# Kernel tuning notes

Measured on AMD Instinct MI355X. Metric: run time of the kernel, lower is better.

## Reference

```python
import jax, jax.numpy as jnp
import numpy as np

B, T = 2, 5            # num_frames MUST equal 5 (Embedding(5, channel) pos table)
C, CTX_C, DH = 384, 128, 64   # channel, context_channel, dim_head (lucidrains default, heads=1)
HW = [(80, 80), (40, 40), (20, 20), (10, 10)]
NS = 4
SCALE = DH ** -0.5


def _xavier(k, shape):
    fan_out, fan_in = shape[-2], shape[-1]
    lim = (6.0 / (fan_in + fan_out)) ** 0.5
    return jax.random.uniform(k, shape, jnp.float32, -lim, lim)


def setup_inputs() -> dict:
    key = jax.random.key(0)
    ks = iter(jax.random.split(key, 40))
    inp = {}
    for i, (h, w) in enumerate(HW):
        inp[f"fmap{i}"] = jax.random.normal(next(ks), (B * T, C, h, w), jnp.float32)
        inp[f"pos{i}"] = jax.random.normal(next(ks), (B, T, C, h, w), jnp.float32)
        inp[f"audio{i}"] = jax.random.normal(next(ks), (B * T, CTX_C), jnp.float32)
    inp["ctx_proj_w"] = _xavier(next(ks), (NS, C, CTX_C))
    inp["ctx_proj_b"] = jnp.zeros((NS, C), jnp.float32)
    inp["pos_emb"] = jax.random.normal(next(ks), (NS, 5, C), jnp.float32)  # Embedding(5, channel) per stage
    inp["qk_w"] = _xavier(next(ks), (NS, DH, C))
    inp["ctx_qk_w"] = _xavier(next(ks), (NS, DH, C))
    inp["v_w"] = _xavier(next(ks), (NS, DH, C))
    inp["ctx_v_w"] = _xavier(next(ks), (NS, DH, C))
    inp["out_w"] = _xavier(next(ks), (NS, C, DH))
    inp["out_b"] = jnp.zeros((NS, C), jnp.float32)
    inp["ctx_out_w"] = _xavier(next(ks), (NS, C, DH))
    inp["ctx_out_b"] = jnp.zeros((NS, C), jnp.float32)
    inp["batch_size"] = B
    inp["num_frames"] = T
    return inp


def _stage(x, pos, audio, Wp, bp, pe, Wqk, Wcqk, Wv, Wcv, Wo, bo, Wco, bco, batch_size):
    bt, c, h, w = x.shape
    # audio projection 128 -> 384
    a = audio @ Wp.T + bp                                  # (bt, C)
    # 'hw' reshape: tokens = H*W per (batch*frame)
    xf = x.reshape(bt, c, h * w).transpose(0, 2, 1)        # (bt, hw, C)
    vp = pos.reshape(bt, c, h * w).transpose(0, 2, 1)      # (bt, hw, C)
    ctx = a[:, None, :]                                    # (bt, 1, C)
    cp = jnp.tile(pe, (batch_size, 1))[:, None, :]         # (bt, 1, C); bt == 5*batch_size
    # bidirectional cross-attention (heads=1), pos added to QK inputs only
    qk = (xf + vp) @ Wqk.T                                 # (bt, hw, DH)
    v = xf @ Wv.T                                          # (bt, hw, DH)
    cqk = (ctx + cp) @ Wcqk.T                              # (bt, 1, DH)
    cv = ctx @ Wcv.T                                       # (bt, 1, DH)
    sim = jnp.einsum('bid,bjd->bij', qk, cqk) * SCALE      # (bt, hw, 1) shared similarity
    attn = jax.nn.softmax(sim, axis=-1)                    # video attends over context (j)
    ctx_attn = jax.nn.softmax(sim, axis=-2)                # context attends over video (i)
    out = jnp.einsum('bij,bjd->bid', attn, cv) @ Wo.T + bo         # (bt, hw, C)
    ctx_out = jnp.einsum('bij,bid->bjd', ctx_attn, v) @ Wco.T + bco  # (bt, 1, C)
    vout = out.transpose(0, 2, 1).reshape(bt, c, h, w)
    aout = ctx_out[:, 0, :]                                # (bt, C)
    return vout, aout


def reference(fmap0, fmap1, fmap2, fmap3, audio0, audio1, audio2, audio3,
              pos0, pos1, pos2, pos3,
              ctx_proj_w, ctx_proj_b, pos_emb, qk_w, ctx_qk_w, v_w, ctx_v_w,
              out_w, out_b, ctx_out_w, ctx_out_b, batch_size, num_frames):
    fmaps = (fmap0, fmap1, fmap2, fmap3)
    poss = (pos0, pos1, pos2, pos3)
    audios = (audio0, audio1, audio2, audio3)
    vouts, aouts = [], []
    for i in range(NS):
        vo, ao = _stage(fmaps[i], poss[i], audios[i],
                        ctx_proj_w[i], ctx_proj_b[i], pos_emb[i],
                        qk_w[i], ctx_qk_w[i], v_w[i], ctx_v_w[i],
                        out_w[i], out_b[i], ctx_out_w[i], ctx_out_b[i], batch_size)
        vouts.append(vo)
        aouts.append(ao)
    return tuple(vouts) + tuple(aouts)
```

## Files before the change

kernel.cpp:

```cpp
#include <hip/hip_runtime.h>

#define BT 10
#define CC 384
#define DH 64
#define CTXC 128
#define NS 4
#define SCALE_F 0.125f

#define VOFF0 0
#define VOFF1 24576000
#define VOFF2 30720000
#define VOFF3 32256000
#define AOUT_OFF 32640000

struct Params {
  const float* fmap0; const float* fmap1; const float* fmap2; const float* fmap3;
  const float* pos0;  const float* pos1;  const float* pos2;  const float* pos3;
  const float* audio0;const float* audio1;const float* audio2;const float* audio3;
  const float* ctx_proj_w; const float* ctx_proj_b; const float* pos_emb;
  const float* qk_w; const float* ctx_qk_w; const float* v_w; const float* ctx_v_w;
  const float* out_w; const float* out_b; const float* ctx_out_w; const float* ctx_out_b;
  float* out;
  float* r;
  float* outvec;
  float* xw;
  float* simbuf;
};

__device__ __forceinline__ int hw_of(int s){ return s==0?6400: s==1?1600: s==2?400:100; }
__device__ __forceinline__ int simoff(int s){ return s==0?0: s==1?64000: s==2?80000:84000; }
__device__ __forceinline__ const float* fm_of(const Params& P, int s){ return s==0?P.fmap0: s==1?P.fmap1: s==2?P.fmap2:P.fmap3; }
__device__ __forceinline__ const float* po_of(const Params& P, int s){ return s==0?P.pos0: s==1?P.pos1: s==2?P.pos2:P.pos3; }
__device__ __forceinline__ const float* au_of(const Params& P, int s){ return s==0?P.audio0: s==1?P.audio1: s==2?P.audio2:P.audio3; }

__global__ __launch_bounds__(384) void k_pre(Params P) {
  const int s = blockIdx.x / BT, b = blockIdx.x % BT;
  const int tid = threadIdx.x;
  __shared__ float aud[CTXC], ctxv[CC], ctxpe[CC], cqk[DH], cvv[DH];
  const float* audio = au_of(P, s);
  if (tid < CTXC) aud[tid] = audio[b*CTXC + tid];
  __syncthreads();
  {
    float acc = P.ctx_proj_b[s*CC + tid];
    const float* wrow = P.ctx_proj_w + (size_t)(s*CC + tid)*CTXC;
    #pragma unroll 8
    for (int k = 0; k < CTXC; ++k) acc += wrow[k]*aud[k];
    ctxv[tid] = acc;
    ctxpe[tid] = acc + P.pos_emb[(s*5 + (b%5))*CC + tid];
  }
  __syncthreads();
  if (tid < DH) {
    float q = 0.f, v = 0.f;
    const float* wq = P.ctx_qk_w + (size_t)(s*DH + tid)*CC;
    const float* wv = P.ctx_v_w  + (size_t)(s*DH + tid)*CC;
    #pragma unroll 4
    for (int c = 0; c < CC; ++c) { q += wq[c]*ctxpe[c]; v += wv[c]*ctxv[c]; }
    cqk[tid] = q; cvv[tid] = v;
  }
  __syncthreads();
  {
    float rr = 0.f, ov = P.out_b[s*CC + tid];
    const float* wqk = P.qk_w + (size_t)s*DH*CC + tid;
    const float* wo  = P.out_w + (size_t)(s*CC + tid)*DH;
    #pragma unroll 4
    for (int d = 0; d < DH; ++d) { rr += wqk[(size_t)d*CC]*cqk[d]; ov += wo[d]*cvv[d]; }
    P.r[(s*BT+b)*CC + tid] = rr * SCALE_F;
    P.outvec[(s*BT+b)*CC + tid] = ov;
  }
}

__global__ __launch_bounds__(256) void k_sim(Params P) {
  const int bid = blockIdx.x;
  int s, b, chunk, part, HW;
  if (bid < 560)      { s=0; int l=bid;     b=l/56; int r2=l%56; chunk=r2>>3; part=r2&7; HW=6400; }
  else if (bid < 720) { s=1; int l=bid-560; b=l/16; int r2=l%16; chunk=r2>>3; part=r2&7; HW=1600; }
  else if (bid < 800) { s=2; int l=bid-720; b=l>>3; part=l&7; chunk=0; HW=400; }
  else                { s=3; int l=bid-800; b=l>>3; part=l&7; chunk=0; HW=100; }
  const int tid = threadIdx.x;
  const int c0 = part*48;
  const int hw4 = HW >> 2;

  __shared__ float rs[48];
  if (tid < 48) rs[tid] = P.r[(s*BT+b)*CC + c0 + tid];
  __syncthreads();

  const int i4 = chunk*256 + tid;
  if (i4 < hw4) {
    const float4* xp = (const float4*)(fm_of(P, s) + ((size_t)b*CC + c0)*HW) + i4;
    const float4* pp = (const float4*)(po_of(P, s) + ((size_t)b*CC + c0)*HW) + i4;
    float4 acc = {0.f, 0.f, 0.f, 0.f};
    #pragma unroll 8
    for (int c = 0; c < 48; ++c) {
      const float4 x = xp[(size_t)c*hw4];
      const float4 p = pp[(size_t)c*hw4];
      const float rc = rs[c];
      acc.x += (x.x + p.x) * rc;
      acc.y += (x.y + p.y) * rc;
      acc.z += (x.z + p.z) * rc;
      acc.w += (x.w + p.w) * rc;
    }
    float* dst = P.simbuf + simoff(s) + b*HW + i4*4;
    atomicAdd(dst + 0, acc.x);
    atomicAdd(dst + 1, acc.y);
    atomicAdd(dst + 2, acc.z);
    atomicAdd(dst + 3, acc.w);
  }
}

__global__ __launch_bounds__(256) void k_softmax(Params P) {
  const int s = blockIdx.x / BT, b = blockIdx.x % BT;
  const int HW = hw_of(s);
  float* sim = P.simbuf + simoff(s) + b*HW;
  const int tid = threadIdx.x;
  const int wid = tid >> 6, lane = tid & 63;
  __shared__ float red[4], red2[4];

  float m = -1e30f;
  for (int i = tid; i < HW; i += 256) m = fmaxf(m, sim[i]);
  #pragma unroll
  for (int off = 32; off; off >>= 1) m = fmaxf(m, __shfl_down(m, off));
  if (lane == 0) red[wid] = m;
  __syncthreads();
  if (tid == 0) { float mm = red[0]; for (int w2 = 1; w2 < 4; ++w2) mm = fmaxf(mm, red[w2]); red[0] = mm; }
  __syncthreads();
  m = red[0];

  float sum = 0.f;
  for (int i = tid; i < HW; i += 256) { float e = expf(sim[i] - m); sim[i] = e; sum += e; }
  #pragma unroll
  for (int off = 32; off; off >>= 1) sum += __shfl_down(sum, off);
  if (lane == 0) red2[wid] = sum;
  __syncthreads();
  if (tid == 0) { float ss = red2[0]; for (int w2 = 1; w2 < 4; ++w2) ss += red2[w2]; red2[0] = ss; }
  __syncthreads();
  const float invS = 1.f / red2[0];

  for (int i = tid; i < HW; i += 256) sim[i] *= invS;
}

__global__ __launch_bounds__(256) void k_xw(Params P) {
  const int bid = blockIdx.x;
  const int sb = bid / 96, ct = bid % 96;
  const int s = sb / BT, b = sb % BT;
  const int HW = hw_of(s);
  const int wid = threadIdx.x >> 6, lane = threadIdx.x & 63;
  const int c = ct*4 + wid;
  const float* xrow = fm_of(P, s) + ((size_t)(b*CC + c))*HW;
  const float* wrow = P.simbuf + simoff(s) + b*HW;
  float ax=0.f, ay=0.f, az=0.f, aw=0.f;
  #pragma unroll 4
  for (int i0 = lane*4; i0 < HW; i0 += 256) {
    const float4 x4 = *(const float4*)(xrow + i0);
    const float4 w4 = *(const float4*)(wrow + i0);
    ax += x4.x*w4.x; ay += x4.y*w4.y; az += x4.z*w4.z; aw += x4.w*w4.w;
  }
  float acc = (ax + ay) + (az + aw);
  #pragma unroll
  for (int off = 32; off; off >>= 1) acc += __shfl_down(acc, off);
  if (lane == 0) P.xw[(s*BT+b)*CC + c] = acc;
}

__global__ __launch_bounds__(384) void k_post(Params P) {
  const int s = blockIdx.x / BT, b = blockIdx.x % BT;
  const int tid = threadIdx.x;
  __shared__ float xws[CC], ctxo[DH];
  xws[tid] = P.xw[(s*BT+b)*CC + tid];
  __syncthreads();
  if (tid < DH) {
    float acc = 0.f;
    const float* wv = P.v_w + (size_t)(s*DH + tid)*CC;
    #pragma unroll 4
    for (int c = 0; c < CC; ++c) acc += wv[c]*xws[c];
    ctxo[tid] = acc;
  }
  __syncthreads();
  float ao = P.ctx_out_b[s*CC + tid];
  const float* wco = P.ctx_out_w + (size_t)(s*CC + tid)*DH;
  #pragma unroll 4
  for (int d = 0; d < DH; ++d) ao += wco[d]*ctxo[d];
  P.out[(size_t)AOUT_OFF + (s*BT+b)*CC + tid] = ao;
}

template<int F4PR, int VOFF, int OVOFF>
__device__ __forceinline__ void fill_one(const Params& P, int idx) {
  const int row = idx / F4PR;
  const float val = P.outvec[OVOFF + row];
  const float4 v4 = {val, val, val, val};
  ((float4*)(P.out + VOFF))[idx] = v4;
}

__global__ __launch_bounds__(256) void k_fill(Params P) {
  const int gid = blockIdx.x * 256 + threadIdx.x;
  if (blockIdx.x < 24000)      fill_one<1600, VOFF0, 0>    (P, gid);
  else if (blockIdx.x < 30000) fill_one< 400, VOFF1, 3840> (P, gid - 24000*256);
  else if (blockIdx.x < 31500) fill_one< 100, VOFF2, 7680> (P, gid - 30000*256);
  else                         fill_one<  25, VOFF3, 11520>(P, gid - 31500*256);
}

extern "C" void kernel_launch(void* const* d_in, const int* in_sizes, int n_in,
                              void* d_out, int out_size, void* d_ws, size_t ws_size,
                              hipStream_t stream) {
  Params P;
  P.fmap0 = (const float*)d_in[0];  P.pos0 = (const float*)d_in[1];  P.audio0 = (const float*)d_in[2];
  P.fmap1 = (const float*)d_in[3];  P.pos1 = (const float*)d_in[4];  P.audio1 = (const float*)d_in[5];
  P.fmap2 = (const float*)d_in[6];  P.pos2 = (const float*)d_in[7];  P.audio2 = (const float*)d_in[8];
  P.fmap3 = (const float*)d_in[9];  P.pos3 = (const float*)d_in[10]; P.audio3 = (const float*)d_in[11];
  P.ctx_proj_w = (const float*)d_in[12]; P.ctx_proj_b = (const float*)d_in[13];
  P.pos_emb = (const float*)d_in[14];
  P.qk_w = (const float*)d_in[15];  P.ctx_qk_w = (const float*)d_in[16];
  P.v_w = (const float*)d_in[17];   P.ctx_v_w = (const float*)d_in[18];
  P.out_w = (const float*)d_in[19]; P.out_b = (const float*)d_in[20];
  P.ctx_out_w = (const float*)d_in[21]; P.ctx_out_b = (const float*)d_in[22];
  P.out = (float*)d_out;

  float* ws = (float*)d_ws;
  P.r      = ws;
  P.outvec = ws + 15360;
  P.xw     = ws + 30720;
  P.simbuf = ws + 46080;

  hipMemsetAsync(P.simbuf, 0, 85000*sizeof(float), stream);
  k_pre    <<<NS*BT, 384, 0, stream>>>(P);
  k_sim    <<<880,   256, 0, stream>>>(P);
  k_softmax<<<NS*BT, 256, 0, stream>>>(P);
  k_xw     <<<3840,  256, 0, stream>>>(P);
  k_post   <<<NS*BT, 384, 0, stream>>>(P);
  k_fill   <<<31875, 256, 0, stream>>>(P);
}
```

Baseline: 471.5 us.

## Split sim kernel across arrays and finer channel parts, parallelize small GEMVs

```diff
diff --git a/kernel.cpp b/kernel.cpp
--- a/kernel.cpp
+++ b/kernel.cpp
@@ -37,24 +37,33 @@
   const int s = blockIdx.x / BT, b = blockIdx.x % BT;
   const int tid = threadIdx.x;
   __shared__ float aud[CTXC], ctxv[CC], ctxpe[CC], cqk[DH], cvv[DH];
+  __shared__ float pq[6][DH], pvv[6][DH];
   const float* audio = au_of(P, s);
   if (tid < CTXC) aud[tid] = audio[b*CTXC + tid];
   __syncthreads();
   {
     float acc = P.ctx_proj_b[s*CC + tid];
     const float* wrow = P.ctx_proj_w + (size_t)(s*CC + tid)*CTXC;
-    #pragma unroll 8
+    #pragma unroll 16
     for (int k = 0; k < CTXC; ++k) acc += wrow[k]*aud[k];
     ctxv[tid] = acc;
     ctxpe[tid] = acc + P.pos_emb[(s*5 + (b%5))*CC + tid];
   }
   __syncthreads();
+  {
+    const int g = tid >> 6, oid = tid & 63;
+    float q = 0.f, v = 0.f;
+    const float* wq = P.ctx_qk_w + (size_t)(s*DH + oid)*CC + g*64;
+    const float* wv = P.ctx_v_w  + (size_t)(s*DH + oid)*CC + g*64;
+    #pragma unroll 8
+    for (int c = 0; c < 64; ++c) { q += wq[c]*ctxpe[g*64+c]; v += wv[c]*ctxv[g*64+c]; }
+    pq[g][oid] = q; pvv[g][oid] = v;
+  }
+  __syncthreads();
   if (tid < DH) {
     float q = 0.f, v = 0.f;
-    const float* wq = P.ctx_qk_w + (size_t)(s*DH + tid)*CC;
-    const float* wv = P.ctx_v_w  + (size_t)(s*DH + tid)*CC;
-    #pragma unroll 4
-    for (int c = 0; c < CC; ++c) { q += wq[c]*ctxpe[c]; v += wv[c]*ctxv[c]; }
+    #pragma unroll
+    for (int g2 = 0; g2 < 6; ++g2) { q += pq[g2][tid]; v += pvv[g2][tid]; }
     cqk[tid] = q; cvv[tid] = v;
   }
   __syncthreads();
@@ -62,7 +71,7 @@
     float rr = 0.f, ov = P.out_b[s*CC + tid];
     const float* wqk = P.qk_w + (size_t)s*DH*CC + tid;
     const float* wo  = P.out_w + (size_t)(s*CC + tid)*DH;
-    #pragma unroll 4
+    #pragma unroll 8
     for (int d = 0; d < DH; ++d) { rr += wqk[(size_t)d*CC]*cqk[d]; ov += wo[d]*cvv[d]; }
     P.r[(s*BT+b)*CC + tid] = rr * SCALE_F;
     P.outvec[(s*BT+b)*CC + tid] = ov;
@@ -71,33 +80,33 @@
 
 __global__ __launch_bounds__(256) void k_sim(Params P) {
   const int bid = blockIdx.x;
-  int s, b, chunk, part, HW;
-  if (bid < 560)      { s=0; int l=bid;     b=l/56; int r2=l%56; chunk=r2>>3; part=r2&7; HW=6400; }
-  else if (bid < 720) { s=1; int l=bid-560; b=l/16; int r2=l%16; chunk=r2>>3; part=r2&7; HW=1600; }
-  else if (bid < 800) { s=2; int l=bid-720; b=l>>3; part=l&7; chunk=0; HW=400; }
-  else                { s=3; int l=bid-800; b=l>>3; part=l&7; chunk=0; HW=100; }
-  const int tid = threadIdx.x;
-  const int c0 = part*48;
+  int s, b, chunk, part, arr, HW;
+  if (bid < 2240)      { s=0; int l=bid;      arr=l&1; l>>=1; part=l&15; l>>=4; chunk=l%7; b=l/7; HW=6400; }
+  else if (bid < 2880) { s=1; int l=bid-2240; arr=l&1; l>>=1; part=l&15; l>>=4; chunk=l&1; b=l>>1; HW=1600; }
+  else if (bid < 3200) { s=2; int l=bid-2880; arr=l&1; l>>=1; part=l&15; b=l>>4; chunk=0; HW=400; }
+  else                 { s=3; int l=bid-3200; arr=l&1; l>>=1; part=l&15; b=l>>4; chunk=0; HW=100; }
+  const int tid = threadIdx.x;
+  const int c0 = part*24;
   const int hw4 = HW >> 2;
 
-  __shared__ float rs[48];
-  if (tid < 48) rs[tid] = P.r[(s*BT+b)*CC + c0 + tid];
+  __shared__ float rs[24];
+  if (tid < 24) rs[tid] = P.r[(s*BT+b)*CC + c0 + tid];
   __syncthreads();
 
   const int i4 = chunk*256 + tid;
   if (i4 < hw4) {
-    const float4* xp = (const float4*)(fm_of(P, s) + ((size_t)b*CC + c0)*HW) + i4;
-    const float4* pp = (const float4*)(po_of(P, s) + ((size_t)b*CC + c0)*HW) + i4;
+    const float* src = arr ? po_of(P, s) : fm_of(P, s);
+    const float4* ap = (const float4*)(src + ((size_t)b*CC + c0)*HW) + i4;
     float4 acc = {0.f, 0.f, 0.f, 0.f};
-    #pragma unroll 8
-    for (int c = 0; c < 48; ++c) {
-      const float4 x = xp[(size_t)c*hw4];
-      const float4 p = pp[(size_t)c*hw4];
-      const float rc = rs[c];
-      acc.x += (x.x + p.x) * rc;
-      acc.y += (x.y + p.y) * rc;
-      acc.z += (x.z + p.z) * rc;
-      acc.w += (x.w + p.w) * rc;
+    for (int cb = 0; cb < 24; cb += 8) {
+      float4 v[8];
+      #pragma unroll
+      for (int u = 0; u < 8; ++u) v[u] = ap[(size_t)(cb+u)*hw4];
+      #pragma unroll
+      for (int u = 0; u < 8; ++u) {
+        const float rc = rs[cb+u];
+        acc.x += v[u].x*rc; acc.y += v[u].y*rc; acc.z += v[u].z*rc; acc.w += v[u].w*rc;
+      }
     }
     float* dst = P.simbuf + simoff(s) + b*HW + i4*4;
     atomicAdd(dst + 0, acc.x);
@@ -147,14 +156,20 @@
   const int c = ct*4 + wid;
   const float* xrow = fm_of(P, s) + ((size_t)(b*CC + c))*HW;
   const float* wrow = P.simbuf + simoff(s) + b*HW;
-  float ax=0.f, ay=0.f, az=0.f, aw=0.f;
-  #pragma unroll 4
-  for (int i0 = lane*4; i0 < HW; i0 += 256) {
-    const float4 x4 = *(const float4*)(xrow + i0);
-    const float4 w4 = *(const float4*)(wrow + i0);
-    ax += x4.x*w4.x; ay += x4.y*w4.y; az += x4.z*w4.z; aw += x4.w*w4.w;
-  }
-  float acc = (ax + ay) + (az + aw);
+  float acc = 0.f;
+  for (int i0 = lane*4; i0 < HW; i0 += 1024) {
+    float4 x4[4], w4[4];
+    #pragma unroll
+    for (int u = 0; u < 4; ++u) {
+      const int idx = i0 + u*256;
+      if (idx < HW) { x4[u] = *(const float4*)(xrow + idx); w4[u] = *(const float4*)(wrow + idx); }
+    }
+    #pragma unroll
+    for (int u = 0; u < 4; ++u) {
+      const int idx = i0 + u*256;
+      if (idx < HW) acc += x4[u].x*w4[u].x + x4[u].y*w4[u].y + x4[u].z*w4[u].z + x4[u].w*w4[u].w;
+    }
+  }
   #pragma unroll
   for (int off = 32; off; off >>= 1) acc += __shfl_down(acc, off);
   if (lane == 0) P.xw[(s*BT+b)*CC + c] = acc;
@@ -163,20 +178,28 @@
 __global__ __launch_bounds__(384) void k_post(Params P) {
   const int s = blockIdx.x / BT, b = blockIdx.x % BT;
   const int tid = threadIdx.x;
-  __shared__ float xws[CC], ctxo[DH];
+  __shared__ float xws[CC], ctxo[DH], pc[6][DH];
   xws[tid] = P.xw[(s*BT+b)*CC + tid];
   __syncthreads();
+  {
+    const int g = tid >> 6, oid = tid & 63;
+    float a = 0.f;
+    const float* wv = P.v_w + (size_t)(s*DH + oid)*CC + g*64;
+    #pragma unroll 8
+    for (int c = 0; c < 64; ++c) a += wv[c]*xws[g*64+c];
+    pc[g][oid] = a;
+  }
+  __syncthreads();
   if (tid < DH) {
-    float acc = 0.f;
-    const float* wv = P.v_w + (size_t)(s*DH + tid)*CC;
-    #pragma unroll 4
-    for (int c = 0; c < CC; ++c) acc += wv[c]*xws[c];
-    ctxo[tid] = acc;
+    float a = 0.f;
+    #pragma unroll
+    for (int g2 = 0; g2 < 6; ++g2) a += pc[g2][tid];
+    ctxo[tid] = a;
   }
   __syncthreads();
   float ao = P.ctx_out_b[s*CC + tid];
   const float* wco = P.ctx_out_w + (size_t)(s*CC + tid)*DH;
-  #pragma unroll 4
+  #pragma unroll 8
   for (int d = 0; d < DH; ++d) ao += wco[d]*ctxo[d];
   P.out[(size_t)AOUT_OFF + (s*BT+b)*CC + tid] = ao;
 }
@@ -221,7 +244,7 @@
 
   hipMemsetAsync(P.simbuf, 0, 85000*sizeof(float), stream);
   k_pre    <<<NS*BT, 384, 0, stream>>>(P);
-  k_sim    <<<880,   256, 0, stream>>>(P);
+  k_sim    <<<3520,  256, 0, stream>>>(P);
   k_softmax<<<NS*BT, 256, 0, stream>>>(P);
   k_xw     <<<3840,  256, 0, stream>>>(P);
   k_post   <<<NS*BT, 384, 0, stream>>>(P);
```

After: 441.0 us. 6.5% less time.
